# Kernel tuning notes

Measured on AMD Instinct MI355X. Metric: run time of the kernel, lower is better.

The kernel has to match this reference:

```python
import jax, jax.numpy as jnp
import numpy as np

MARGIN = 1.0
SOFT = False
EPS = 1e-4


def setup_inputs() -> dict:
    key = jax.random.key(0)
    k1, k2 = jax.random.split(key)
    embeddings = jax.random.normal(k1, (256, 128), dtype=jnp.float32)
    labels = jax.random.randint(k2, (256,), 0, 16, dtype=jnp.int64)
    return {"embeddings": embeddings, "labels": labels}


def _pdist(A):
    prod = A @ A.T                      # [n, n]
    norm = jnp.diag(prod)[:, None]      # [n, 1]
    res = jnp.clip(norm + norm.T - 2.0 * prod, 0.0)
    return jnp.sqrt(jnp.clip(res, EPS))


def reference(embeddings, labels):
    d = _pdist(embeddings)                               # [n, n]
    n = d.shape[0]
    pos = (labels[:, None] == labels[None, :]).astype(d.dtype) - jnp.eye(n, dtype=d.dtype)

    # dist_diff[i, j, k] = d[i, k] - d[i, j]
    dist_diff = d[:, None, :] - d[:, :, None]            # [n, n, n]
    # M[i, j, k] = pos[i, k] * (1 - pos[i, j])
    M = pos[:, None, :] * (1.0 - pos)[:, :, None]        # [n, n, n]
    mask = M * (dist_diff < 0).astype(d.dtype)           # [n, n, n]
    mask_final = mask.sum(axis=1) > 0                    # [n, n]

    # masked maximum over j (semi-hard negatives exist)
    axis_min = dist_diff.min(axis=1, keepdims=True)
    neg_outside = ((dist_diff - axis_min) * mask).max(axis=1) + axis_min[:, 0, :]
    # masked minimum over j (fallback: easiest negative)
    axis_max = dist_diff.max(axis=1, keepdims=True)
    neg_inside = ((dist_diff - axis_max) * M).min(axis=1) + axis_max[:, 0, :]

    semi_hard = jnp.where(mask_final, neg_outside, neg_inside)  # [n, n]
    if SOFT:
        loss_mat = jnp.log1p(jnp.exp(semi_hard))
    else:
        loss_mat = semi_hard + MARGIN
    return jnp.sum(jax.nn.relu(pos * loss_mat)) / jnp.sum(pos)
```

## Files before the change

### kernel.cpp

```cpp
#include <hip/hip_runtime.h>
#include <float.h>
#include <math.h>

#define N 256
#define D 128
#define EPS_F 1e-4f
#define MARGIN_F 1.0f

__global__ __launch_bounds__(N) void triplet_fused_kernel(
    const float* __restrict__ E,
    const int*   __restrict__ lab,
    float* __restrict__ out)
{
    __shared__ __align__(16) float ei[D];
    __shared__ __align__(16) float drow[N];
    __shared__ __align__(16) int   labs[N];
    __shared__ float red[8];

    const int i = blockIdx.x;
    const int k = threadIdx.x;

    if (k < D / 4) {
        ((float4*)ei)[k] = ((const float4*)(E + (size_t)i * D))[k];
    }
    labs[k] = lab[k];
    __syncthreads();

    const float4* __restrict__ Ek = (const float4*)(E + (size_t)k * D);
    float s = 0.0f;
#pragma unroll
    for (int t = 0; t < D / 4; ++t) {
        float4 a = ((const float4*)ei)[t];
        float4 b = Ek[t];
        float dx = a.x - b.x, dy = a.y - b.y, dz = a.z - b.z, dw = a.w - b.w;
        s += dx * dx + dy * dy + dz * dz + dw * dw;
    }
    const float dik = sqrtf(fmaxf(s, EPS_F));
    drow[k] = dik;
    __syncthreads();

    const int li = labs[i];
    const int lk = labs[k];

    float minS = FLT_MAX;
    float maxN = -FLT_MAX;
    int   matches = 0;
#pragma unroll 4
    for (int jj = 0; jj < N / 4; ++jj) {
        const float4 d4 = ((const float4*)drow)[jj];
        const int4   l4 = ((const int4*)labs)[jj];
        const int j0 = jj * 4;
        {
            const bool nz = (l4.x != li) || (j0 + 0 == i);
            maxN = fmaxf(maxN, nz ? d4.x : -FLT_MAX);
            minS = fminf(minS, (nz && d4.x > dik) ? d4.x : FLT_MAX);
            matches += (l4.x == lk);
        }
        {
            const bool nz = (l4.y != li) || (j0 + 1 == i);
            maxN = fmaxf(maxN, nz ? d4.y : -FLT_MAX);
            minS = fminf(minS, (nz && d4.y > dik) ? d4.y : FLT_MAX);
            matches += (l4.y == lk);
        }
        {
            const bool nz = (l4.z != li) || (j0 + 2 == i);
            maxN = fmaxf(maxN, nz ? d4.z : -FLT_MAX);
            minS = fminf(minS, (nz && d4.z > dik) ? d4.z : FLT_MAX);
            matches += (l4.z == lk);
        }
        {
            const bool nz = (l4.w != li) || (j0 + 3 == i);
            maxN = fmaxf(maxN, nz ? d4.w : -FLT_MAX);
            minS = fminf(minS, (nz && d4.w > dik) ? d4.w : FLT_MAX);
            matches += (l4.w == lk);
        }
    }

    const bool ispos = (lk == li) && (k != i);
    const float chosen = (minS < FLT_MAX) ? minS : maxN;
    const float term = ispos ? fmaxf(dik - chosen + MARGIN_F, 0.0f) : 0.0f;
    const float cntk = (float)(matches - 1);

    float ts = term, cs = cntk;
    for (int off = 32; off > 0; off >>= 1) {
        ts += __shfl_down(ts, off);
        cs += __shfl_down(cs, off);
    }
    const int lane = k & 63;
    const int wid  = k >> 6;
    if (lane == 0) { red[wid] = ts; red[4 + wid] = cs; }
    __syncthreads();
    if (k == 0) {
        const float blocksum = red[0] + red[1] + red[2] + red[3];
        const float cnt      = red[4] + red[5] + red[6] + red[7];
        atomicAdd(out, blocksum / cnt);
    }
}

extern "C" void kernel_launch(void* const* d_in, const int* in_sizes, int n_in,
                              void* d_out, int out_size, void* d_ws, size_t ws_size,
                              hipStream_t stream) {
    const float* E   = (const float*)d_in[0];
    const int*   lab = (const int*)d_in[1];
    float* out = (float*)d_out;

    triplet_fused_kernel<<<N, N, 0, stream>>>(E, lab, out);
}
```

Baseline: 71.97 us.

## Stage full embedding matrix in LDS via async global_load_lds and simplify reductions

Each block now copies the whole 256x128 embedding matrix into shared memory with direct global-to-LDS loads using an XOR swizzle, then computes distances from LDS instead of strided global reads. The negative max is found with a wave reduction, the semi-hard min loop reads a single pre-masked distance array, and the positive-pair count comes from a shared label histogram instead of a per-thread 256-step match loop. The 128 KB LDS footprint limits occupancy to one block per CU, and every block reloads the full matrix.

```diff
diff --git a/kernel.cpp b/kernel.cpp
--- a/kernel.cpp
+++ b/kernel.cpp
@@ -4,6 +4,7 @@
 
 #define N 256
 #define D 128
+#define NU 32
 #define EPS_F 1e-4f
 #define MARGIN_F 1.0f
 
@@ -12,88 +13,93 @@
     const int*   __restrict__ lab,
     float* __restrict__ out)
 {
-    __shared__ __align__(16) float ei[D];
-    __shared__ __align__(16) float drow[N];
-    __shared__ __align__(16) int   labs[N];
+    __shared__ __align__(16) float Es[N * D];
+    __shared__ __align__(16) float sd[N];
     __shared__ float red[8];
+    __shared__ int   hist[16];
 
     const int i = blockIdx.x;
     const int k = threadIdx.x;
 
-    if (k < D / 4) {
-        ((float4*)ei)[k] = ((const float4*)(E + (size_t)i * D))[k];
-    }
-    labs[k] = lab[k];
-    __syncthreads();
+    if (k < 16) hist[k] = 0;
 
-    const float4* __restrict__ Ek = (const float4*)(E + (size_t)k * D);
-    float s = 0.0f;
+    {
+        const int r0 = k >> 5;
+        const int t0 = (k & 31) ^ r0;
+        const float* gbase = E + (size_t)r0 * D + t0 * 4;
+        float* lbase = Es + (size_t)k * 4;
 #pragma unroll
-    for (int t = 0; t < D / 4; ++t) {
-        float4 a = ((const float4*)ei)[t];
-        float4 b = Ek[t];
-        float dx = a.x - b.x, dy = a.y - b.y, dz = a.z - b.z, dw = a.w - b.w;
-        s += dx * dx + dy * dy + dz * dz + dw * dw;
-    }
-    const float dik = sqrtf(fmaxf(s, EPS_F));
-    drow[k] = dik;
-    __syncthreads();
-
-    const int li = labs[i];
-    const int lk = labs[k];
-
-    float minS = FLT_MAX;
-    float maxN = -FLT_MAX;
-    int   matches = 0;
-#pragma unroll 4
-    for (int jj = 0; jj < N / 4; ++jj) {
-        const float4 d4 = ((const float4*)drow)[jj];
-        const int4   l4 = ((const int4*)labs)[jj];
-        const int j0 = jj * 4;
-        {
-            const bool nz = (l4.x != li) || (j0 + 0 == i);
-            maxN = fmaxf(maxN, nz ? d4.x : -FLT_MAX);
-            minS = fminf(minS, (nz && d4.x > dik) ? d4.x : FLT_MAX);
-            matches += (l4.x == lk);
-        }
-        {
-            const bool nz = (l4.y != li) || (j0 + 1 == i);
-            maxN = fmaxf(maxN, nz ? d4.y : -FLT_MAX);
-            minS = fminf(minS, (nz && d4.y > dik) ? d4.y : FLT_MAX);
-            matches += (l4.y == lk);
-        }
-        {
-            const bool nz = (l4.z != li) || (j0 + 2 == i);
-            maxN = fmaxf(maxN, nz ? d4.z : -FLT_MAX);
-            minS = fminf(minS, (nz && d4.z > dik) ? d4.z : FLT_MAX);
-            matches += (l4.z == lk);
-        }
-        {
-            const bool nz = (l4.w != li) || (j0 + 3 == i);
-            maxN = fmaxf(maxN, nz ? d4.w : -FLT_MAX);
-            minS = fminf(minS, (nz && d4.w > dik) ? d4.w : FLT_MAX);
-            matches += (l4.w == lk);
+        for (int it = 0; it < 32; ++it) {
+            __builtin_amdgcn_global_load_lds(
+                (const __attribute__((address_space(1))) void*)(gbase + it * 1024),
+                (__attribute__((address_space(3))) void*)(lbase + it * 1024),
+                16, 0, 0);
         }
     }
 
+    const int lk = lab[k];
+    const int li = lab[i];
+
+    __syncthreads();
+
+    atomicAdd(&hist[lk], 1);
+
+    const float4* Ev = (const float4*)Es;
+    const int bi = i * NU, si = i & 7;
+    const int bk = k * NU, sk = k & 7;
+    float sx = 0.f, sy = 0.f, sz = 0.f, sw = 0.f;
+#pragma unroll
+    for (int t = 0; t < NU; ++t) {
+        const float4 a = Ev[bi + (t ^ si)];
+        const float4 b = Ev[bk + (t ^ sk)];
+        const float dx = a.x - b.x, dy = a.y - b.y;
+        const float dz = a.z - b.z, dw = a.w - b.w;
+        sx += dx * dx; sy += dy * dy; sz += dz * dz; sw += dw * dw;
+    }
+    const float dik = sqrtf(fmaxf((sx + sy) + (sz + sw), EPS_F));
+
+    const bool nz = (lk != li) || (k == i);
+    sd[k] = nz ? dik : FLT_MAX;
+
+    float nd = nz ? dik : -FLT_MAX;
+#pragma unroll
+    for (int off = 32; off > 0; off >>= 1)
+        nd = fmaxf(nd, __shfl_down(nd, off));
+    const int lane = k & 63;
+    const int wid  = k >> 6;
+    if (lane == 0) red[wid] = nd;
+
+    __syncthreads();
+
+    const float maxN = fmaxf(fmaxf(red[0], red[1]), fmaxf(red[2], red[3]));
+
+    float m0 = FLT_MAX, m1 = FLT_MAX, m2 = FLT_MAX, m3 = FLT_MAX;
+    const float4* sv = (const float4*)sd;
+#pragma unroll 8
+    for (int jj = 0; jj < N / 4; ++jj) {
+        const float4 v = sv[jj];
+        m0 = fminf(m0, v.x > dik ? v.x : FLT_MAX);
+        m1 = fminf(m1, v.y > dik ? v.y : FLT_MAX);
+        m2 = fminf(m2, v.z > dik ? v.z : FLT_MAX);
+        m3 = fminf(m3, v.w > dik ? v.w : FLT_MAX);
+    }
+    const float minS = fminf(fminf(m0, m1), fminf(m2, m3));
+
     const bool ispos = (lk == li) && (k != i);
     const float chosen = (minS < FLT_MAX) ? minS : maxN;
-    const float term = ispos ? fmaxf(dik - chosen + MARGIN_F, 0.0f) : 0.0f;
-    const float cntk = (float)(matches - 1);
+    float ts = ispos ? fmaxf(dik - chosen + MARGIN_F, 0.f) : 0.f;
+#pragma unroll
+    for (int off = 32; off > 0; off >>= 1)
+        ts += __shfl_down(ts, off);
+    if (lane == 0) red[4 + wid] = ts;
+    __syncthreads();
 
-    float ts = term, cs = cntk;
-    for (int off = 32; off > 0; off >>= 1) {
-        ts += __shfl_down(ts, off);
-        cs += __shfl_down(cs, off);
-    }
-    const int lane = k & 63;
-    const int wid  = k >> 6;
-    if (lane == 0) { red[wid] = ts; red[4 + wid] = cs; }
-    __syncthreads();
     if (k == 0) {
-        const float blocksum = red[0] + red[1] + red[2] + red[3];
-        const float cnt      = red[4] + red[5] + red[6] + red[7];
-        atomicAdd(out, blocksum / cnt);
+        const float bs = red[4] + red[5] + red[6] + red[7];
+        int cnt = 0;
+#pragma unroll
+        for (int l = 0; l < 16; ++l) cnt += hist[l] * (hist[l] - 1);
+        atomicAdd(out, bs / (float)cnt);
     }
 }
 
```

After: 62.08 us. 13.7% less time.
